# Kernel tuning notes

Hardware: AMD Instinct MI355X
Metric: run time of the kernel (lower is better)

## Reference

```python
import jax, jax.numpy as jnp
import numpy as np

IN, H1, H2, H3, H4, OUT = 512, 2048, 2048, 1024, 512, 1


def setup_inputs() -> dict:
    key = jax.random.key(0)
    ks = jax.random.split(key, 12)
    def lin(k, fan_in, fan_out):
        # torch Linear default init: U(-1/sqrt(fan_in), 1/sqrt(fan_in))
        bound = 1.0 / np.sqrt(fan_in)
        k1, k2 = jax.random.split(k)
        W = jax.random.uniform(k1, (fan_out, fan_in), jnp.float32, -bound, bound)
        b = jax.random.uniform(k2, (fan_out,), jnp.float32, -bound, bound)
        return W, b
    x = jax.random.normal(ks[0], (16384, IN), jnp.float32)
    cross_w = jnp.ones((IN,), jnp.float32)   # init.constant_(1.0)
    cross_b = jnp.zeros((IN,), jnp.float32)  # init.constant_(0.0)
    W1, b1 = lin(ks[1], IN, H1)
    W2, b2 = lin(ks[2], H1, H2)
    W3, b3 = lin(ks[3], H2, H3)
    W4, b4 = lin(ks[4], H3, H4)
    Wo, bo = lin(ks[5], H4, OUT)
    return {"x": x, "cross_w": cross_w, "cross_b": cross_b,
            "W1": W1, "b1": b1, "W2": W2, "b2": b2,
            "W3": W3, "b3": b3, "W4": W4, "b4": b4,
            "Wo": Wo, "bo": bo}


def reference(x, cross_w, cross_b, W1, b1, W2, b2, W3, b3, W4, b4, Wo, bo):
    # Cross layer: bmm(x0[...,None], x[...,None,:]) . w == x0 * (x . w)
    # (mathematically identical, avoids the O(f^2) outer product)
    xw = x @ cross_w                         # [B]
    h = x * xw[:, None] + cross_b + x        # [B, IN]
    h = jax.nn.relu(h @ W1.T + b1)           # [B, H1]
    h = jax.nn.relu(h @ W2.T + b2)           # [B, H2]
    h = jax.nn.relu(h @ W3.T + b3)           # [B, H3]
    h = jax.nn.relu(h @ W4.T + b4)           # [B, H4]
    return h @ Wo.T + bo                     # [B, OUT]
```

## Files before the change

### kernel.cpp

```cpp
#include <hip/hip_runtime.h>


#define BK 64

typedef __bf16 bf16x8 __attribute__((ext_vector_type(8)));
typedef float  f32x4  __attribute__((ext_vector_type(4)));
typedef unsigned short u16x4 __attribute__((ext_vector_type(4)));

__device__ __forceinline__ unsigned short f2bf(float f) {
    unsigned int u = __builtin_bit_cast(unsigned int, f);
    u += 0x7fffu + ((u >> 16) & 1u);
    return (unsigned short)(u >> 16);
}
__device__ __forceinline__ float bf2f(unsigned short h) {
    unsigned int u = ((unsigned int)h) << 16;
    return __builtin_bit_cast(float, u);
}

__device__ __forceinline__ void async16(const void* g, void* l) {
    __builtin_amdgcn_global_load_lds(
        (const __attribute__((address_space(1))) unsigned int*)g,
        (__attribute__((address_space(3))) unsigned int*)l,
        16, 0, 0);
}

template<int BN>
__global__ __launch_bounds__(256, 2)
void gemm_bt_bias_relu(const unsigned short* __restrict__ A,
                       const unsigned short* __restrict__ B,
                       const float* __restrict__ bias,
                       unsigned short* __restrict__ C,
                       int M, int N, int K)
{
    constexpr int JT = BN / 32;
    __shared__ __align__(16) unsigned short As[128 * BK];
    __shared__ __align__(16) unsigned short Bs[2 * BN * BK];

    const int tid  = threadIdx.x;
    const int lane = tid & 63;
    const int wave = tid >> 6;
    const int quad = lane >> 4;
    const int l16  = lane & 15;

    const int bm = blockIdx.x * 128;
    const int bn = blockIdx.y * BN;
    const int wm = (wave & 1) * 64;
    const int wn = (wave >> 1) * (BN / 2);

    const int lrow = tid >> 3;
    const int gcol = ((tid & 7) ^ (lrow & 7)) * 8;

    const unsigned short* gaBase = A + (size_t)(bm + lrow) * K + gcol;
    const unsigned short* gbBase = B + (size_t)(bn + lrow) * K + gcol;

    unsigned short* lA = As + tid * 8;

    const int xa = l16 & 7;
    const unsigned short* As_w = As + (wm + l16) * BK;
    const int c0 = (quad ^ xa) * 8;
    const int c1 = ((quad ^ 4) ^ xa) * 8;

    f32x4 acc[4][JT] = {};
    bf16x8 areg[4];

    auto compute = [&](const unsigned short* Bsb) {
        const unsigned short* Bw = Bsb + (wn + l16) * BK;
#pragma unroll
        for (int kk = 0; kk < 2; ++kk) {
            const int cs = kk ? c1 : c0;
            bf16x8 af[4], bfr[JT];
#pragma unroll
            for (int i = 0; i < 4; ++i)  af[i]  = *(const bf16x8*)(As_w + i * 16 * BK + cs);
#pragma unroll
            for (int j = 0; j < JT; ++j) bfr[j] = *(const bf16x8*)(Bw + j * 16 * BK + cs);
#pragma unroll
            for (int i = 0; i < 4; ++i)
#pragma unroll
                for (int j = 0; j < JT; ++j)
                    acc[i][j] = __builtin_amdgcn_mfma_f32_16x16x32_bf16(
                        af[i], bfr[j], acc[i][j], 0, 0, 0);
        }
    };

    const int nk = K / BK;

#pragma unroll
    for (int i = 0; i < 4; ++i)
        areg[i] = *(const bf16x8*)(gaBase + (size_t)(i * 32) * K);
    {
        unsigned short* lB0 = Bs + tid * 8;
#pragma unroll
        for (int i = 0; i < JT; ++i)
            async16(gbBase + (size_t)(i * 32) * K, lB0 + i * 2048);
    }
#pragma unroll
    for (int i = 0; i < 4; ++i)
        *(bf16x8*)(lA + i * 2048) = areg[i];
    __syncthreads();

    for (int k = 0; k < nk - 1; ++k) {
        const size_t k0n = (size_t)(k + 1) * BK;
#pragma unroll
        for (int i = 0; i < 4; ++i)
            areg[i] = *(const bf16x8*)(gaBase + (size_t)(i * 32) * K + k0n);
        unsigned short* lBn = Bs + ((k + 1) & 1) * (BN * BK) + tid * 8;
#pragma unroll
        for (int i = 0; i < JT; ++i)
            async16(gbBase + (size_t)(i * 32) * K + k0n, lBn + i * 2048);

        compute(Bs + (k & 1) * (BN * BK));
        __syncthreads();
#pragma unroll
        for (int i = 0; i < 4; ++i)
            *(bf16x8*)(lA + i * 2048) = areg[i];
        __syncthreads();
    }
    compute(Bs + ((nk - 1) & 1) * (BN * BK));

    float bv[JT];
#pragma unroll
    for (int j = 0; j < JT; ++j) bv[j] = bias[bn + wn + j * 16 + l16];

#pragma unroll
    for (int i = 0; i < 4; ++i) {
        const int row0 = bm + wm + i * 16 + quad * 4;
#pragma unroll
        for (int j = 0; j < JT; ++j) {
            const int col = bn + wn + j * 16 + l16;
#pragma unroll
            for (int r = 0; r < 4; ++r) {
                float v = acc[i][j][r] + bv[j];
                v = fmaxf(v, 0.0f);
                C[(size_t)(row0 + r) * N + col] = f2bf(v);
            }
        }
    }
}

__global__ __launch_bounds__(256)
void prep_kernel(const float* __restrict__ x, const float* __restrict__ cw,
                 const float* __restrict__ cb, unsigned short* __restrict__ h0,
                 const float* __restrict__ s1, const float* __restrict__ s2,
                 const float* __restrict__ s3, const float* __restrict__ s4,
                 unsigned short* __restrict__ d1, unsigned short* __restrict__ d2,
                 unsigned short* __restrict__ d3, unsigned short* __restrict__ d4)
{
    const int b = blockIdx.x;
    if (b < 7680) {
        long t = (long)b * 256 + threadIdx.x;
        const float* s; unsigned short* d; long off;
        if (t < 262144L)       { s = s1; d = d1; off = t; }
        else if (t < 1310720L) { s = s2; d = d2; off = t - 262144L; }
        else if (t < 1835008L) { s = s3; d = d3; off = t - 1310720L; }
        else                   { s = s4; d = d4; off = t - 1835008L; }
        f32x4 f = *(const f32x4*)(s + off * 4);
        u16x4 o;
#pragma unroll
        for (int i = 0; i < 4; ++i) o[i] = f2bf(f[i]);
        *(u16x4*)(d + off * 4) = o;
    } else {
        const int row  = (b - 7680) * 4 + (threadIdx.x >> 6);
        const int lane = threadIdx.x & 63;
        const float* xr = x + (size_t)row * 512;
        float xv[8];
        float s = 0.f;
#pragma unroll
        for (int i = 0; i < 8; ++i) {
            const int c = lane + i * 64;
            xv[i] = xr[c];
            s += xv[i] * cw[c];
        }
#pragma unroll
        for (int off = 32; off > 0; off >>= 1) s += __shfl_down(s, off, 64);
        s = __shfl(s, 0, 64);
        unsigned short* hr = h0 + (size_t)row * 512;
#pragma unroll
        for (int i = 0; i < 8; ++i) {
            const int c = lane + i * 64;
            hr[c] = f2bf(xv[i] * s + cb[c] + xv[i]);
        }
    }
}

__global__ __launch_bounds__(256)
void final_dot(const unsigned short* __restrict__ h4, const float* __restrict__ Wo,
               const float* __restrict__ bo, float* __restrict__ out)
{
    const int row  = blockIdx.x * 4 + (threadIdx.x >> 6);
    const int lane = threadIdx.x & 63;
    const unsigned short* hr = h4 + (size_t)row * 512;
    float s = 0.f;
#pragma unroll
    for (int i = 0; i < 8; ++i) {
        const int c = lane + i * 64;
        s += bf2f(hr[c]) * Wo[c];
    }
#pragma unroll
    for (int off = 32; off > 0; off >>= 1) s += __shfl_down(s, off, 64);
    if (lane == 0) out[row] = s + bo[0];
}

extern "C" void kernel_launch(void* const* d_in, const int* in_sizes, int n_in,
                              void* d_out, int out_size, void* d_ws, size_t ws_size,
                              hipStream_t stream)
{
    const float* x  = (const float*)d_in[0];
    const float* cw = (const float*)d_in[1];
    const float* cb = (const float*)d_in[2];
    const float* W1 = (const float*)d_in[3];  const float* b1 = (const float*)d_in[4];
    const float* W2 = (const float*)d_in[5];  const float* b2 = (const float*)d_in[6];
    const float* W3 = (const float*)d_in[7];  const float* b3 = (const float*)d_in[8];
    const float* W4 = (const float*)d_in[9];  const float* b4 = (const float*)d_in[10];
    const float* Wo = (const float*)d_in[11]; const float* bo = (const float*)d_in[12];
    float* out = (float*)d_out;

    char* p = (char*)d_ws;
    unsigned short* wb1 = (unsigned short*)p; p += (size_t)2048 * 512  * 2;
    unsigned short* wb2 = (unsigned short*)p; p += (size_t)2048 * 2048 * 2;
    unsigned short* wb3 = (unsigned short*)p; p += (size_t)1024 * 2048 * 2;
    unsigned short* wb4 = (unsigned short*)p; p += (size_t)512  * 1024 * 2;
    unsigned short* actA = (unsigned short*)p; p += (size_t)16384 * 2048 * 2;
    unsigned short* actB = (unsigned short*)p;

    prep_kernel<<<11776, 256, 0, stream>>>(x, cw, cb, actA,
                                           W1, W2, W3, W4, wb1, wb2, wb3, wb4);

    gemm_bt_bias_relu<256><<<dim3(128, 8), 256, 0, stream>>>(actA, wb1, b1, actB, 16384, 2048, 512);
    gemm_bt_bias_relu<256><<<dim3(128, 8), 256, 0, stream>>>(actB, wb2, b2, actA, 16384, 2048, 2048);
    gemm_bt_bias_relu<256><<<dim3(128, 4), 256, 0, stream>>>(actA, wb3, b3, actB, 16384, 1024, 2048);
    gemm_bt_bias_relu<128><<<dim3(128, 4), 256, 0, stream>>>(actB, wb4, b4, actA, 16384, 512, 1024);
    final_dot<<<4096, 256, 0, stream>>>(actA, Wo, bo, out);
}
```

Before: 375.5 us.

## Fuse output head into last GEMM, simplify GEMM pipeline, swap grid order

The last hidden GEMM now reduces each row of its ReLU output against Wo in registers and atomically adds the partial sums into the output. The output is pre-seeded with the bias in the prep kernel, which removes the separate final_dot pass and the write and reread of h4. The GEMM main loop drops its double-buffered, register-staged prefetch and becomes a single-buffer loop that async-loads A and B straight to LDS, with a sync before and after compute. The grid is transposed so the N-tiles sharing one A row-block are adjacent, which is meant to improve L2 reuse of A but removes the overlap of loads with compute.

```diff
diff --git a/kernel.cpp b/kernel.cpp
--- a/kernel.cpp
+++ b/kernel.cpp
@@ -11,10 +11,6 @@
     unsigned int u = __builtin_bit_cast(unsigned int, f);
     u += 0x7fffu + ((u >> 16) & 1u);
     return (unsigned short)(u >> 16);
-}
-__device__ __forceinline__ float bf2f(unsigned short h) {
-    unsigned int u = ((unsigned int)h) << 16;
-    return __builtin_bit_cast(float, u);
 }
 
 __device__ __forceinline__ void async16(const void* g, void* l) {
@@ -34,7 +30,7 @@
 {
     constexpr int JT = BN / 32;
     __shared__ __align__(16) unsigned short As[128 * BK];
-    __shared__ __align__(16) unsigned short Bs[2 * BN * BK];
+    __shared__ __align__(16) unsigned short Bs[BN * BK];
 
     const int tid  = threadIdx.x;
     const int lane = tid & 63;
@@ -42,8 +38,8 @@
     const int quad = lane >> 4;
     const int l16  = lane & 15;
 
-    const int bm = blockIdx.x * 128;
-    const int bn = blockIdx.y * BN;
+    const int bm = blockIdx.y * 128;
+    const int bn = blockIdx.x * BN;
     const int wm = (wave & 1) * 64;
     const int wn = (wave >> 1) * (BN / 2);
 
@@ -54,17 +50,25 @@
     const unsigned short* gbBase = B + (size_t)(bn + lrow) * K + gcol;
 
     unsigned short* lA = As + tid * 8;
+    unsigned short* lB = Bs + tid * 8;
 
     const int xa = l16 & 7;
     const unsigned short* As_w = As + (wm + l16) * BK;
+    const unsigned short* Bs_w = Bs + (wn + l16) * BK;
     const int c0 = (quad ^ xa) * 8;
     const int c1 = ((quad ^ 4) ^ xa) * 8;
 
     f32x4 acc[4][JT] = {};
-    bf16x8 areg[4];
-
-    auto compute = [&](const unsigned short* Bsb) {
-        const unsigned short* Bw = Bsb + (wn + l16) * BK;
+
+    for (int k0 = 0; k0 < K; k0 += BK) {
+#pragma unroll
+        for (int i = 0; i < 4; ++i)
+            async16(gaBase + (size_t)(i * 32) * K + k0, lA + i * 2048);
+#pragma unroll
+        for (int i = 0; i < JT; ++i)
+            async16(gbBase + (size_t)(i * 32) * K + k0, lB + i * 2048);
+        __syncthreads();
+
 #pragma unroll
         for (int kk = 0; kk < 2; ++kk) {
             const int cs = kk ? c1 : c0;
@@ -72,7 +76,7 @@
 #pragma unroll
             for (int i = 0; i < 4; ++i)  af[i]  = *(const bf16x8*)(As_w + i * 16 * BK + cs);
 #pragma unroll
-            for (int j = 0; j < JT; ++j) bfr[j] = *(const bf16x8*)(Bw + j * 16 * BK + cs);
+            for (int j = 0; j < JT; ++j) bfr[j] = *(const bf16x8*)(Bs_w + j * 16 * BK + cs);
 #pragma unroll
             for (int i = 0; i < 4; ++i)
 #pragma unroll
@@ -80,42 +84,8 @@
                     acc[i][j] = __builtin_amdgcn_mfma_f32_16x16x32_bf16(
                         af[i], bfr[j], acc[i][j], 0, 0, 0);
         }
-    };
-
-    const int nk = K / BK;
-
-#pragma unroll
-    for (int i = 0; i < 4; ++i)
-        areg[i] = *(const bf16x8*)(gaBase + (size_t)(i * 32) * K);
-    {
-        unsigned short* lB0 = Bs + tid * 8;
-#pragma unroll
-        for (int i = 0; i < JT; ++i)
-            async16(gbBase + (size_t)(i * 32) * K, lB0 + i * 2048);
-    }
-#pragma unroll
-    for (int i = 0; i < 4; ++i)
-        *(bf16x8*)(lA + i * 2048) = areg[i];
-    __syncthreads();
-
-    for (int k = 0; k < nk - 1; ++k) {
-        const size_t k0n = (size_t)(k + 1) * BK;
-#pragma unroll
-        for (int i = 0; i < 4; ++i)
-            areg[i] = *(const bf16x8*)(gaBase + (size_t)(i * 32) * K + k0n);
-        unsigned short* lBn = Bs + ((k + 1) & 1) * (BN * BK) + tid * 8;
-#pragma unroll
-        for (int i = 0; i < JT; ++i)
-            async16(gbBase + (size_t)(i * 32) * K + k0n, lBn + i * 2048);
-
-        compute(Bs + (k & 1) * (BN * BK));
-        __syncthreads();
-#pragma unroll
-        for (int i = 0; i < 4; ++i)
-            *(bf16x8*)(lA + i * 2048) = areg[i];
-        __syncthreads();
-    }
-    compute(Bs + ((nk - 1) & 1) * (BN * BK));
+        __syncthreads();
+    }
 
     float bv[JT];
 #pragma unroll
@@ -132,6 +102,104 @@
                 float v = acc[i][j][r] + bv[j];
                 v = fmaxf(v, 0.0f);
                 C[(size_t)(row0 + r) * N + col] = f2bf(v);
+            }
+        }
+    }
+}
+
+__global__ __launch_bounds__(256, 2)
+void gemm_bt_head(const unsigned short* __restrict__ A,
+                  const unsigned short* __restrict__ B,
+                  const float* __restrict__ bias,
+                  const float* __restrict__ Wo,
+                  float* __restrict__ out,
+                  int M, int N, int K)
+{
+    constexpr int BN = 128;
+    constexpr int JT = 4;
+    __shared__ __align__(16) unsigned short As[128 * BK];
+    __shared__ __align__(16) unsigned short Bs[BN * BK];
+
+    const int tid  = threadIdx.x;
+    const int lane = tid & 63;
+    const int wave = tid >> 6;
+    const int quad = lane >> 4;
+    const int l16  = lane & 15;
+
+    const int bm = blockIdx.y * 128;
+    const int bn = blockIdx.x * BN;
+    const int wm = (wave & 1) * 64;
+    const int wn = (wave >> 1) * 64;
+
+    const int lrow = tid >> 3;
+    const int gcol = ((tid & 7) ^ (lrow & 7)) * 8;
+
+    const unsigned short* gaBase = A + (size_t)(bm + lrow) * K + gcol;
+    const unsigned short* gbBase = B + (size_t)(bn + lrow) * K + gcol;
+
+    unsigned short* lA = As + tid * 8;
+    unsigned short* lB = Bs + tid * 8;
+
+    const int xa = l16 & 7;
+    const unsigned short* As_w = As + (wm + l16) * BK;
+    const unsigned short* Bs_w = Bs + (wn + l16) * BK;
+    const int c0 = (quad ^ xa) * 8;
+    const int c1 = ((quad ^ 4) ^ xa) * 8;
+
+    f32x4 acc[4][JT] = {};
+
+    for (int k0 = 0; k0 < K; k0 += BK) {
+#pragma unroll
+        for (int i = 0; i < 4; ++i)
+            async16(gaBase + (size_t)(i * 32) * K + k0, lA + i * 2048);
+#pragma unroll
+        for (int i = 0; i < JT; ++i)
+            async16(gbBase + (size_t)(i * 32) * K + k0, lB + i * 2048);
+        __syncthreads();
+
+#pragma unroll
+        for (int kk = 0; kk < 2; ++kk) {
+            const int cs = kk ? c1 : c0;
+            bf16x8 af[4], bfr[JT];
+#pragma unroll
+            for (int i = 0; i < 4; ++i)  af[i]  = *(const bf16x8*)(As_w + i * 16 * BK + cs);
+#pragma unroll
+            for (int j = 0; j < JT; ++j) bfr[j] = *(const bf16x8*)(Bs_w + j * 16 * BK + cs);
+#pragma unroll
+            for (int i = 0; i < 4; ++i)
+#pragma unroll
+                for (int j = 0; j < JT; ++j)
+                    acc[i][j] = __builtin_amdgcn_mfma_f32_16x16x32_bf16(
+                        af[i], bfr[j], acc[i][j], 0, 0, 0);
+        }
+        __syncthreads();
+    }
+
+    float bv[JT], wov[JT];
+#pragma unroll
+    for (int j = 0; j < JT; ++j) {
+        const int col = bn + wn + j * 16 + l16;
+        bv[j]  = bias[col];
+        wov[j] = Wo[col];
+    }
+
+#pragma unroll
+    for (int i = 0; i < 4; ++i) {
+#pragma unroll
+        for (int r = 0; r < 4; ++r) {
+            float ws = 0.f;
+#pragma unroll
+            for (int j = 0; j < JT; ++j) {
+                float v = acc[i][j][r] + bv[j];
+                v = fmaxf(v, 0.0f);
+                ws += v * wov[j];
+            }
+#pragma unroll
+            for (int off = 8; off > 0; off >>= 1)
+                ws += __shfl_xor(ws, off, 64);
+            if (l16 == 0) {
+                const int row = bm + wm + i * 16 + quad * 4 + r;
+                atomicAdd(&out[row], ws);
             }
         }
     }
@@ -143,7 +211,8 @@
                  const float* __restrict__ s1, const float* __restrict__ s2,
                  const float* __restrict__ s3, const float* __restrict__ s4,
                  unsigned short* __restrict__ d1, unsigned short* __restrict__ d2,
-                 unsigned short* __restrict__ d3, unsigned short* __restrict__ d4)
+                 unsigned short* __restrict__ d3, unsigned short* __restrict__ d4,
+                 const float* __restrict__ bo, float* __restrict__ out)
 {
     const int b = blockIdx.x;
     if (b < 7680) {
@@ -158,7 +227,7 @@
 #pragma unroll
         for (int i = 0; i < 4; ++i) o[i] = f2bf(f[i]);
         *(u16x4*)(d + off * 4) = o;
-    } else {
+    } else if (b < 11776) {
         const int row  = (b - 7680) * 4 + (threadIdx.x >> 6);
         const int lane = threadIdx.x & 63;
         const float* xr = x + (size_t)row * 512;
@@ -179,25 +248,10 @@
             const int c = lane + i * 64;
             hr[c] = f2bf(xv[i] * s + cb[c] + xv[i]);
         }
-    }
-}
-
-__global__ __launch_bounds__(256)
-void final_dot(const unsigned short* __restrict__ h4, const float* __restrict__ Wo,
-               const float* __restrict__ bo, float* __restrict__ out)
-{
-    const int row  = blockIdx.x * 4 + (threadIdx.x >> 6);
-    const int lane = threadIdx.x & 63;
-    const unsigned short* hr = h4 + (size_t)row * 512;
-    float s = 0.f;
-#pragma unroll
-    for (int i = 0; i < 8; ++i) {
-        const int c = lane + i * 64;
-        s += bf2f(hr[c]) * Wo[c];
-    }
-#pragma unroll
-    for (int off = 32; off > 0; off >>= 1) s += __shfl_down(s, off, 64);
-    if (lane == 0) out[row] = s + bo[0];
+    } else {
+        const int t = (b - 11776) * 256 + threadIdx.x;
+        out[t] = bo[0];
+    }
 }
 
 extern "C" void kernel_launch(void* const* d_in, const int* in_sizes, int n_in,
@@ -222,12 +276,12 @@
     unsigned short* actA = (unsigned short*)p; p += (size_t)16384 * 2048 * 2;
     unsigned short* actB = (unsigned short*)p;
 
-    prep_kernel<<<11776, 256, 0, stream>>>(x, cw, cb, actA,
-                                           W1, W2, W3, W4, wb1, wb2, wb3, wb4);
-
-    gemm_bt_bias_relu<256><<<dim3(128, 8), 256, 0, stream>>>(actA, wb1, b1, actB, 16384, 2048, 512);
-    gemm_bt_bias_relu<256><<<dim3(128, 8), 256, 0, stream>>>(actB, wb2, b2, actA, 16384, 2048, 2048);
-    gemm_bt_bias_relu<256><<<dim3(128, 4), 256, 0, stream>>>(actA, wb3, b3, actB, 16384, 1024, 2048);
-    gemm_bt_bias_relu<128><<<dim3(128, 4), 256, 0, stream>>>(actB, wb4, b4, actA, 16384, 512, 1024);
-    final_dot<<<4096, 256, 0, stream>>>(actA, Wo, bo, out);
-}
+    prep_kernel<<<11840, 256, 0, stream>>>(x, cw, cb, actA,
+                                           W1, W2, W3, W4, wb1, wb2, wb3, wb4,
+                                           bo, out);
+
+    gemm_bt_bias_relu<256><<<dim3(8, 128), 256, 0, stream>>>(actA, wb1, b1, actB, 16384, 2048, 512);
+    gemm_bt_bias_relu<256><<<dim3(8, 128), 256, 0, stream>>>(actB, wb2, b2, actA, 16384, 2048, 2048);
+    gemm_bt_bias_relu<256><<<dim3(4, 128), 256, 0, stream>>>(actA, wb3, b3, actB, 16384, 1024, 2048);
+    gemm_bt_head<<<dim3(4, 128), 256, 0, stream>>>(actB, wb4, b4, Wo, out, 16384, 512, 1024);
+}
```

Result: no change. 369.0 us (-1.7%).
